# Kernel optimization log

Measured on AMD Instinct MI355X. Metric: run time of the kernel, lower is better.

## Reference

```python
import jax, jax.numpy as jnp
import numpy as np

N_NODES = 100000


def gcn_conv(x, edge_index, W, b):
    # PyG GCNConv: add self-loops, symmetric deg^-1/2 normalization,
    # linear transform, scatter-add aggregation onto destination nodes.
    src = edge_index[0]
    dst = edge_index[1]
    loops = jnp.arange(N_NODES, dtype=edge_index.dtype)
    src = jnp.concatenate([src, loops])
    dst = jnp.concatenate([dst, loops])
    deg = jax.ops.segment_sum(jnp.ones_like(src, dtype=x.dtype), dst,
                              num_segments=N_NODES)
    dinv = jnp.where(deg > 0, jax.lax.rsqrt(deg), 0.0)  # deg^-1/2, 0 for isolated
    norm = dinv[src] * dinv[dst]                        # [E+N]
    h = x @ W                                           # [N, out]
    msg = h[src] * norm[:, None]                        # [E+N, out]
    out = jax.ops.segment_sum(msg, dst, num_segments=N_NODES)
    return out + b


def setup_inputs() -> dict:
    key = jax.random.key(0)
    k1, k2, k3, k4, k5, k6 = jax.random.split(key, 6)
    in_c, hid_c, out_c = 128, 64, 40
    n_edges = 1_600_000
    x = jax.random.normal(k1, (N_NODES, in_c), dtype=jnp.float32)
    edge_index = jax.random.randint(k2, (2, n_edges), 0, N_NODES, dtype=jnp.int32)
    # Glorot-style init like GCNConv.reset_parameters
    W1 = jax.random.normal(k3, (in_c, hid_c), dtype=jnp.float32) * (1.0 / np.sqrt(in_c))
    b1 = jnp.zeros((hid_c,), dtype=jnp.float32)
    W2 = jax.random.normal(k4, (hid_c, out_c), dtype=jnp.float32) * (1.0 / np.sqrt(hid_c))
    b2 = jnp.zeros((out_c,), dtype=jnp.float32)
    return {"x": x, "edge_index": edge_index, "W1": W1, "b1": b1, "W2": W2, "b2": b2}


def reference(x, edge_index, W1, b1, W2, b2):
    h = jax.nn.relu(gcn_conv(x, edge_index, W1, b1))
    h = gcn_conv(h, edge_index, W2, b2)
    return jax.nn.log_softmax(h, axis=1)
```

## Files before the change

kernel.cpp:

```cpp
#include <hip/hip_runtime.h>
#include <math.h>

#define N_IN  128
#define N_HID 64
#define N_OUT 40

#define BSH   9
#define SZB   512
#define MAXBK 256
#define CAP   9216

typedef __attribute__((ext_vector_type(4))) float f32x4;
typedef __attribute__((ext_vector_type(8))) short bf16x8;

__device__ __forceinline__ unsigned short bf16_of(float x) {
    unsigned b = __float_as_uint(x);
    return (unsigned short)((b + 0x7fffu + ((b >> 16) & 1u)) >> 16);
}
__device__ __forceinline__ unsigned pack_bf16(float lo, float hi) {
    unsigned bl = __float_as_uint(lo), bh = __float_as_uint(hi);
    bl = (bl + 0x7fffu + ((bl >> 16) & 1u)) >> 16;
    bh = (bh + 0x7fffu + ((bh >> 16) & 1u)) & 0xffff0000u;
    return bl | bh;
}
__device__ __forceinline__ float bf_lo(unsigned u) { return __uint_as_float(u << 16); }
__device__ __forceinline__ float bf_hi(unsigned u) { return __uint_as_float(u & 0xffff0000u); }
__device__ __forceinline__ float2 bfup(unsigned u) { return make_float2(bf_lo(u), bf_hi(u)); }
__device__ __forceinline__ float2 f2add(float2 a, float2 b) { return make_float2(a.x + b.x, a.y + b.y); }

#define ACC8(u) { c0 = f2add(c0, bfup(u.x)); c1 = f2add(c1, bfup(u.y)); \
                  c2 = f2add(c2, bfup(u.z)); c3 = f2add(c3, bfup(u.w)); }

__global__ __launch_bounds__(256) void bucket_scatter2(const int* __restrict__ src,
                                                       const int* __restrict__ dst,
                                                       int E, int NBK,
                                                       int* __restrict__ bcnt,
                                                       int* __restrict__ ebuf) {
    __shared__ int h[MAXBK];
    __shared__ int base[MAXBK];
    int chunk = (E + gridDim.x - 1) / gridDim.x;
    int s = blockIdx.x * chunk;
    int e = min(E, s + chunk);
    for (int i = threadIdx.x; i < MAXBK; i += 256) h[i] = 0;
    __syncthreads();
    for (int i = s + threadIdx.x; i < e; i += 256)
        atomicAdd(&h[dst[i] >> BSH], 1);
    __syncthreads();
    for (int i = threadIdx.x; i < NBK; i += 256) {
        int c = h[i];
        base[i] = c ? atomicAdd(&bcnt[i], c) : 0;
    }
    __syncthreads();
    for (int i = threadIdx.x; i < MAXBK; i += 256) h[i] = 0;
    __syncthreads();
    for (int i = s + threadIdx.x; i < e; i += 256) {
        int d = dst[i];
        int b = d >> BSH;
        int lp = base[b] + atomicAdd(&h[b], 1);
        if (lp < CAP)
            ebuf[b * CAP + lp] = (src[i] << BSH) | (d & (SZB - 1));
    }
}

__global__ __launch_bounds__(256) void bucket_finalize2(const int* __restrict__ bcnt,
                                                        const int* __restrict__ ebuf,
                                                        int N,
                                                        int* __restrict__ off,
                                                        int* __restrict__ endo,
                                                        float* __restrict__ dinv,
                                                        int* __restrict__ ssrc) {
    __shared__ int deg[SZB];
    __shared__ int scn[SZB];
    __shared__ int cur[SZB];
    __shared__ int wsum[256];
    __shared__ int sstage[CAP];
    const int b   = blockIdx.x;
    const int cnt = min(bcnt[b], CAP);
    const int e0  = b * CAP;
    const int n0  = b << BSH;
    const int nn  = min(SZB, N - n0);
    const int t   = threadIdx.x;
    deg[t] = 0; deg[t + 256] = 0;
    __syncthreads();
    for (int i = t; i < cnt; i += 256)
        atomicAdd(&deg[ebuf[e0 + i] & (SZB - 1)], 1);
    __syncthreads();
    int a0 = deg[2 * t], a1 = deg[2 * t + 1];
    int v = a0 + a1;
    wsum[t] = v;
    __syncthreads();
    for (int o = 1; o < 256; o <<= 1) {
        int p = (t >= o) ? wsum[t - o] : 0;
        __syncthreads();
        wsum[t] += p;
        __syncthreads();
    }
    int ex = wsum[t] - v;
    scn[2 * t] = ex;       scn[2 * t + 1] = ex + a0;
    cur[2 * t] = ex;       cur[2 * t + 1] = ex + a0;
    __syncthreads();
    for (int i = t; i < nn; i += 256) {
        int st = e0 + scn[i];
        off[n0 + i]  = st;
        endo[n0 + i] = st + deg[i];
        dinv[n0 + i] = rsqrtf((float)(deg[i] + 1));
    }
    for (int i = t; i < cnt; i += 256) {
        int p = ebuf[e0 + i];
        int lp = atomicAdd(&cur[p & (SZB - 1)], 1);
        sstage[lp] = p >> BSH;
    }
    __syncthreads();
    for (int i = t; i < cnt; i += 256) ssrc[e0 + i] = sstage[i];
}

__global__ __launch_bounds__(256) void gemm1_mfma(const float* __restrict__ X,
                                                  const float* __restrict__ W,
                                                  const float* __restrict__ dinv,
                                                  unsigned* __restrict__ T, int nrows) {
    __shared__ unsigned xlds[8192];
    __shared__ unsigned wlds[4096];
    const int t    = threadIdx.x;
    const int row0 = blockIdx.x * 128;

#pragma unroll
    for (int i = 0; i < 16; ++i) {
        int idx = t + i * 256;
        int row = idx >> 5;
        int c4  = idx & 31;
        int gr = row0 + row;
        float4 v = make_float4(0.f, 0.f, 0.f, 0.f);
        if (gr < nrows) v = *(const float4*)&X[(long long)gr * 128 + c4 * 4];
        unsigned p0 = pack_bf16(v.x, v.y);
        unsigned p1 = pack_bf16(v.z, v.w);
        int byte = (row * 256 + c4 * 8) ^ ((row & 7) << 4);
        *(uint2*)((char*)xlds + byte) = make_uint2(p0, p1);
    }
    for (int i = t; i < 128 * 64; i += 256) {
        int k = i >> 6, c = i & 63;
        unsigned short hb = bf16_of(W[i]);
        int byte = (c * 256 + k * 2) ^ ((c & 7) << 4);
        *(unsigned short*)((char*)wlds + byte) = hb;
    }
    __syncthreads();

    const int w    = t >> 6;
    const int l    = t & 63;
    const int lrow = l & 15;
    const int lk   = l >> 4;

    f32x4 acc[2][4];
#pragma unroll
    for (int rt = 0; rt < 2; ++rt)
#pragma unroll
        for (int ct = 0; ct < 4; ++ct) acc[rt][ct] = (f32x4)0.f;

#pragma unroll
    for (int ks = 0; ks < 4; ++ks) {
        bf16x8 af[2], bfr[4];
#pragma unroll
        for (int rt = 0; rt < 2; ++rt) {
            int row = 32 * w + rt * 16 + lrow;
            int byte = (row * 256 + ks * 64 + lk * 16) ^ ((row & 7) << 4);
            af[rt] = *(bf16x8*)((char*)xlds + byte);
        }
#pragma unroll
        for (int ct = 0; ct < 4; ++ct) {
            int col = ct * 16 + lrow;
            int byte = (col * 256 + ks * 64 + lk * 16) ^ ((col & 7) << 4);
            bfr[ct] = *(bf16x8*)((char*)wlds + byte);
        }
#pragma unroll
        for (int rt = 0; rt < 2; ++rt)
#pragma unroll
            for (int ct = 0; ct < 4; ++ct)
                acc[rt][ct] = __builtin_amdgcn_mfma_f32_16x16x32_bf16(
                    af[rt], bfr[ct], acc[rt][ct], 0, 0, 0);
    }
    __syncthreads();
    float* ot = (float*)xlds;
#pragma unroll
    for (int rt = 0; rt < 2; ++rt)
#pragma unroll
        for (int ct = 0; ct < 4; ++ct)
#pragma unroll
            for (int i = 0; i < 4; ++i) {
                int row = 32 * w + rt * 16 + (l >> 4) * 4 + i;
                int col = ct * 16 + (l & 15);
                ot[row * 64 + col] = acc[rt][ct][i];
            }
    __syncthreads();
#pragma unroll
    for (int i = 0; i < 16; ++i) {
        int idx = t + i * 256;
        int row = idx >> 5, u = idx & 31;
        int gr = row0 + row;
        if (gr < nrows) {
            float2 v = *(float2*)&ot[row * 64 + u * 2];
            float dv = dinv[gr];
            T[(long long)gr * 32 + u] = pack_bf16(v.x * dv, v.y * dv);
        }
    }
}

__global__ __launch_bounds__(256) void agg_relu8(const int* __restrict__ off,
                                                 const int* __restrict__ endo,
                                                 const int* __restrict__ ssrc,
                                                 const float* __restrict__ dinv,
                                                 const unsigned* __restrict__ tab,
                                                 const float* __restrict__ bias,
                                                 unsigned* __restrict__ tabC, int N) {
    int node = blockIdx.x * 4 + (threadIdx.x >> 6);
    int lane = threadIdx.x & 63;
    if (node >= N) return;
    const int o  = lane >> 3;
    const int ln = lane & 7;
    int start = off[node], end = endo[node];
    float2 c0 = make_float2(0.f, 0.f), c1 = c0, c2 = c0, c3 = c0;
    for (int j = start; j < end; j += 64) {
        int idx = j + lane;
        int sidx = (idx < end) ? ssrc[idx] : 0;
        int cnt = min(64, end - j);
        int t = 0;
        for (; t + 16 <= cnt; t += 16) {
            int sA = __shfl(sidx, t + o);
            int sB = __shfl(sidx, t + 8 + o);
            uint4 uA = *(const uint4*)(tab + (long long)sA * 32 + 4 * ln);
            uint4 uB = *(const uint4*)(tab + (long long)sB * 32 + 4 * ln);
            ACC8(uA); ACC8(uB);
        }
        for (; t + 8 <= cnt; t += 8) {
            int s = __shfl(sidx, t + o);
            uint4 u = *(const uint4*)(tab + (long long)s * 32 + 4 * ln);
            ACC8(u);
        }
        if (t < cnt) {
            int ei = t + o;
            int s = __shfl(sidx, ei & 63);
            if (ei < cnt) {
                uint4 u = *(const uint4*)(tab + (long long)s * 32 + 4 * ln);
                ACC8(u);
            }
        }
    }
#pragma unroll
    for (int d = 8; d < 64; d <<= 1) {
        c0.x += __shfl_xor(c0.x, d); c0.y += __shfl_xor(c0.y, d);
        c1.x += __shfl_xor(c1.x, d); c1.y += __shfl_xor(c1.y, d);
        c2.x += __shfl_xor(c2.x, d); c2.y += __shfl_xor(c2.y, d);
        c3.x += __shfl_xor(c3.x, d); c3.y += __shfl_xor(c3.y, d);
    }
    if (o == 0) {
        uint4 us = *(const uint4*)(tab + (long long)node * 32 + 4 * ln);
        ACC8(us);
        float dd = dinv[node];
        float4 bb0 = *(const float4*)&bias[8 * ln];
        float4 bb1 = *(const float4*)&bias[8 * ln + 4];
        float v0 = fmaxf(c0.x * dd + bb0.x, 0.f);
        float v1 = fmaxf(c0.y * dd + bb0.y, 0.f);
        float v2 = fmaxf(c1.x * dd + bb0.z, 0.f);
        float v3 = fmaxf(c1.y * dd + bb0.w, 0.f);
        float v4 = fmaxf(c2.x * dd + bb1.x, 0.f);
        float v5 = fmaxf(c2.y * dd + bb1.y, 0.f);
        float v6 = fmaxf(c3.x * dd + bb1.z, 0.f);
        float v7 = fmaxf(c3.y * dd + bb1.w, 0.f);
        uint4 ot;
        ot.x = pack_bf16(v0 * dd, v1 * dd);
        ot.y = pack_bf16(v2 * dd, v3 * dd);
        ot.z = pack_bf16(v4 * dd, v5 * dd);
        ot.w = pack_bf16(v6 * dd, v7 * dd);
        *(uint4*)(tabC + (long long)node * 32 + 4 * ln) = ot;
    }
}

__global__ __launch_bounds__(256) void agg_g8(const int* __restrict__ off,
                                              const int* __restrict__ endo,
                                              const int* __restrict__ ssrc,
                                              const unsigned* __restrict__ tabC,
                                              unsigned* __restrict__ tabG, int N) {
    int node = blockIdx.x * 4 + (threadIdx.x >> 6);
    int lane = threadIdx.x & 63;
    if (node >= N) return;
    const int o  = lane >> 3;
    const int ln = lane & 7;
    int start = off[node], end = endo[node];
    float2 c0 = make_float2(0.f, 0.f), c1 = c0, c2 = c0, c3 = c0;
    for (int j = start; j < end; j += 64) {
        int idx = j + lane;
        int sidx = (idx < end) ? ssrc[idx] : 0;
        int cnt = min(64, end - j);
        int t = 0;
        for (; t + 16 <= cnt; t += 16) {
            int sA = __shfl(sidx, t + o);
            int sB = __shfl(sidx, t + 8 + o);
            uint4 uA = *(const uint4*)(tabC + (long long)sA * 32 + 4 * ln);
            uint4 uB = *(const uint4*)(tabC + (long long)sB * 32 + 4 * ln);
            ACC8(uA); ACC8(uB);
        }
        for (; t + 8 <= cnt; t += 8) {
            int s = __shfl(sidx, t + o);
            uint4 u = *(const uint4*)(tabC + (long long)s * 32 + 4 * ln);
            ACC8(u);
        }
        if (t < cnt) {
            int ei = t + o;
            int s = __shfl(sidx, ei & 63);
            if (ei < cnt) {
                uint4 u = *(const uint4*)(tabC + (long long)s * 32 + 4 * ln);
                ACC8(u);
            }
        }
    }
#pragma unroll
    for (int d = 8; d < 64; d <<= 1) {
        c0.x += __shfl_xor(c0.x, d); c0.y += __shfl_xor(c0.y, d);
        c1.x += __shfl_xor(c1.x, d); c1.y += __shfl_xor(c1.y, d);
        c2.x += __shfl_xor(c2.x, d); c2.y += __shfl_xor(c2.y, d);
        c3.x += __shfl_xor(c3.x, d); c3.y += __shfl_xor(c3.y, d);
    }
    if (o == 0) {
        uint4 us = *(const uint4*)(tabC + (long long)node * 32 + 4 * ln);
        ACC8(us);
        uint4 ot;
        ot.x = pack_bf16(c0.x, c0.y);
        ot.y = pack_bf16(c1.x, c1.y);
        ot.z = pack_bf16(c2.x, c2.y);
        ot.w = pack_bf16(c3.x, c3.y);
        *(uint4*)(tabG + (long long)node * 32 + 4 * ln) = ot;
    }
}

__global__ __launch_bounds__(256) void gemm2_mfma(const unsigned* __restrict__ tabG,
                                                  const float* __restrict__ W2,
                                                  const float* __restrict__ b2,
                                                  const float* __restrict__ dinv,
                                                  float* __restrict__ outp, int nrows) {
    __shared__ unsigned glds[4096];
    __shared__ unsigned wlds[1536];
    const int t    = threadIdx.x;
    const int row0 = blockIdx.x * 128;

#pragma unroll
    for (int i = 0; i < 4; ++i) {
        int idx = t + i * 256;
        int row = idx >> 3;
        int c4  = idx & 7;
        int gr = row0 + row;
        uint4 v = make_uint4(0, 0, 0, 0);
        if (gr < nrows) v = *(const uint4*)(tabG + (long long)gr * 32 + c4 * 4);
        int byte = (row * 128 + c4 * 16) ^ ((row & 7) << 4);
        *(uint4*)((char*)glds + byte) = v;
    }
    for (int i = t; i < 48 * 64; i += 256) {
        int c = i >> 6, k = i & 63;
        unsigned short hb = (c < N_OUT) ? bf16_of(W2[k * N_OUT + c]) : (unsigned short)0;
        int byte = (c * 128 + k * 2) ^ ((c & 7) << 4);
        *(unsigned short*)((char*)wlds + byte) = hb;
    }
    __syncthreads();

    const int w    = t >> 6;
    const int l    = t & 63;
    const int lrow = l & 15;
    const int lk   = l >> 4;

    f32x4 acc[2][3];
#pragma unroll
    for (int rt = 0; rt < 2; ++rt)
#pragma unroll
        for (int ct = 0; ct < 3; ++ct) acc[rt][ct] = (f32x4)0.f;

#pragma unroll
    for (int ks = 0; ks < 2; ++ks) {
        bf16x8 af[2], bfr[3];
#pragma unroll
        for (int rt = 0; rt < 2; ++rt) {
            int row = 32 * w + rt * 16 + lrow;
            int byte = (row * 128 + ks * 64 + lk * 16) ^ ((row & 7) << 4);
            af[rt] = *(bf16x8*)((char*)glds + byte);
        }
#pragma unroll
        for (int ct = 0; ct < 3; ++ct) {
            int col = ct * 16 + lrow;
            int byte = (col * 128 + ks * 64 + lk * 16) ^ ((col & 7) << 4);
            bfr[ct] = *(bf16x8*)((char*)wlds + byte);
        }
#pragma unroll
        for (int rt = 0; rt < 2; ++rt)
#pragma unroll
            for (int ct = 0; ct < 3; ++ct)
                acc[rt][ct] = __builtin_amdgcn_mfma_f32_16x16x32_bf16(
                    af[rt], bfr[ct], acc[rt][ct], 0, 0, 0);
    }

    const int q    = l >> 4;
    const int lcol = l & 15;
    float bb0 = b2[lcol];
    float bb1 = b2[16 + lcol];
    float bb2 = (lcol < 8) ? b2[32 + lcol] : 0.f;
#pragma unroll
    for (int rt = 0; rt < 2; ++rt)
#pragma unroll
        for (int i = 0; i < 4; ++i) {
            int rl = 32 * w + rt * 16 + q * 4 + i;
            int gr = row0 + rl;
            bool ok = gr < nrows;
            float dv = ok ? dinv[gr] : 0.f;
            float v0 = acc[rt][0][i] * dv + bb0;
            float v1 = acc[rt][1][i] * dv + bb1;
            float v2 = (lcol < 8) ? acc[rt][2][i] * dv + bb2 : -INFINITY;
            float m = fmaxf(fmaxf(v0, v1), v2);
            m = fmaxf(m, __shfl_xor(m, 1));
            m = fmaxf(m, __shfl_xor(m, 2));
            m = fmaxf(m, __shfl_xor(m, 4));
            m = fmaxf(m, __shfl_xor(m, 8));
            float ex = __expf(v0 - m) + __expf(v1 - m) + ((lcol < 8) ? __expf(v2 - m) : 0.f);
            ex += __shfl_xor(ex, 1);
            ex += __shfl_xor(ex, 2);
            ex += __shfl_xor(ex, 4);
            ex += __shfl_xor(ex, 8);
            float ls = logf(ex);
            if (ok) {
                long long base = (long long)gr * N_OUT;
                outp[base + lcol]      = v0 - m - ls;
                outp[base + 16 + lcol] = v1 - m - ls;
                if (lcol < 8) outp[base + 32 + lcol] = v2 - m - ls;
            }
        }
}

extern "C" void kernel_launch(void* const* d_in, const int* in_sizes, int n_in,
                              void* d_out, int out_size, void* d_ws, size_t ws_size,
                              hipStream_t stream) {
    const float* x  = (const float*)d_in[0];
    const int*   ei = (const int*)d_in[1];
    const float* W1 = (const float*)d_in[2];
    const float* b1 = (const float*)d_in[3];
    const float* W2 = (const float*)d_in[4];
    const float* b2 = (const float*)d_in[5];
    float* out = (float*)d_out;

    const int N = in_sizes[0] / N_IN;
    const int E = in_sizes[1] / 2;
    const int* src = ei;
    const int* dst = ei + E;
    const int NBK = (N + SZB - 1) >> BSH;

    int*      bcnt = (int*)d_ws;
    int*      off  = bcnt + MAXBK;
    int*      endo = off + N;
    float*    dinv = (float*)(endo + N);
    int*      ssrc = (int*)(dinv + N);
    unsigned* tabA = (unsigned*)(ssrc + (size_t)NBK * CAP);
    unsigned* tabC = tabA + (size_t)N * 32;
    unsigned* tabG = tabC + (size_t)N * 32;
    int*      ebuf = (int*)tabA;

    hipMemsetAsync(bcnt, 0, MAXBK * sizeof(int), stream);

    bucket_scatter2<<<512, 256, 0, stream>>>(src, dst, E, NBK, bcnt, ebuf);
    bucket_finalize2<<<NBK, 256, 0, stream>>>(bcnt, ebuf, N, off, endo, dinv, ssrc);

    gemm1_mfma<<<(N + 127) / 128, 256, 0, stream>>>(x, W1, dinv, tabA, N);
    agg_relu8<<<(N + 3) / 4, 256, 0, stream>>>(off, endo, ssrc, dinv, tabA, b1, tabC, N);

    agg_g8<<<(N + 3) / 4, 256, 0, stream>>>(off, endo, ssrc, tabC, tabG, N);
    gemm2_mfma<<<(N + 127) / 128, 256, 0, stream>>>(tabG, W2, b2, dinv, out, N);
}
```

Before: 179.0 us.

## Sort nodes by degree within buckets and aggregate with 8 lanes per node

The finalize kernel now counting-sorts nodes by in-degree inside each 512-node bucket and writes a packed per-node record (start, end, node id, dinv). Both aggregation kernels switch from one 64-lane wavefront per node, with shuffles and cross-lane reductions, to 8 lanes per node, 8 nodes per wavefront. Each 8-lane group walks its own edges two at a time, and wavefront divergence stays low because neighbouring nodes have similar degree. This removes the shuffle reductions and the idle lanes on low-degree nodes. The cost is less memory-level parallelism per node and extra sorting work in finalize.

```diff
diff --git a/kernel.cpp b/kernel.cpp
--- a/kernel.cpp
+++ b/kernel.cpp
@@ -65,14 +65,14 @@
 __global__ __launch_bounds__(256) void bucket_finalize2(const int* __restrict__ bcnt,
                                                         const int* __restrict__ ebuf,
                                                         int N,
-                                                        int* __restrict__ off,
-                                                        int* __restrict__ endo,
                                                         float* __restrict__ dinv,
-                                                        int* __restrict__ ssrc) {
+                                                        int* __restrict__ ssrc,
+                                                        int4* __restrict__ sinfo) {
     __shared__ int deg[SZB];
     __shared__ int scn[SZB];
     __shared__ int cur[SZB];
     __shared__ int wsum[256];
+    __shared__ int db[128];
     __shared__ int sstage[CAP];
     const int b   = blockIdx.x;
     const int cnt = min(bcnt[b], CAP);
@@ -99,11 +99,30 @@
     scn[2 * t] = ex;       scn[2 * t + 1] = ex + a0;
     cur[2 * t] = ex;       cur[2 * t + 1] = ex + a0;
     __syncthreads();
+    for (int i = t; i < nn; i += 256)
+        dinv[n0 + i] = rsqrtf((float)(deg[i] + 1));
+    if (t < 128) db[t] = 0;
+    __syncthreads();
+    for (int i = t; i < nn; i += 256)
+        atomicAdd(&db[min(deg[i], 127)], 1);
+    __syncthreads();
+    int hv = (t < 128) ? db[t] : 0;
+    wsum[t] = hv;
+    __syncthreads();
+    for (int o = 1; o < 128; o <<= 1) {
+        int p = (t >= o) ? wsum[t - o] : 0;
+        __syncthreads();
+        wsum[t] += p;
+        __syncthreads();
+    }
+    if (t < 128) db[t] = wsum[t] - hv;
+    __syncthreads();
     for (int i = t; i < nn; i += 256) {
+        int dg = deg[i];
+        int r  = atomicAdd(&db[min(dg, 127)], 1);
         int st = e0 + scn[i];
-        off[n0 + i]  = st;
-        endo[n0 + i] = st + deg[i];
-        dinv[n0 + i] = rsqrtf((float)(deg[i] + 1));
+        sinfo[n0 + r] = make_int4(st, st + dg, n0 + i,
+                                  __float_as_int(rsqrtf((float)(dg + 1))));
     }
     for (int i = t; i < cnt; i += 256) {
         int p = ebuf[e0 + i];
@@ -203,59 +222,33 @@
     }
 }
 
-__global__ __launch_bounds__(256) void agg_relu8(const int* __restrict__ off,
-                                                 const int* __restrict__ endo,
-                                                 const int* __restrict__ ssrc,
-                                                 const float* __restrict__ dinv,
-                                                 const unsigned* __restrict__ tab,
-                                                 const float* __restrict__ bias,
-                                                 unsigned* __restrict__ tabC, int N) {
-    int node = blockIdx.x * 4 + (threadIdx.x >> 6);
-    int lane = threadIdx.x & 63;
-    if (node >= N) return;
-    const int o  = lane >> 3;
-    const int ln = lane & 7;
-    int start = off[node], end = endo[node];
+__global__ __launch_bounds__(256) void agg_relu_o(const int4* __restrict__ sinfo,
+                                                  const int* __restrict__ ssrc,
+                                                  const unsigned* __restrict__ tab,
+                                                  const float* __restrict__ bias,
+                                                  unsigned* __restrict__ tabC, int N) {
+    int gidx = blockIdx.x * 32 + (threadIdx.x >> 3);
+    int ol   = threadIdx.x & 7;
+    int4 si = (gidx < N) ? sinfo[gidx] : make_int4(0, 0, 0, 0);
+    int j = si.x, end = si.y;
+    const unsigned* tp = tab + 4 * ol;
     float2 c0 = make_float2(0.f, 0.f), c1 = c0, c2 = c0, c3 = c0;
-    for (int j = start; j < end; j += 64) {
-        int idx = j + lane;
-        int sidx = (idx < end) ? ssrc[idx] : 0;
-        int cnt = min(64, end - j);
-        int t = 0;
-        for (; t + 16 <= cnt; t += 16) {
-            int sA = __shfl(sidx, t + o);
-            int sB = __shfl(sidx, t + 8 + o);
-            uint4 uA = *(const uint4*)(tab + (long long)sA * 32 + 4 * ln);
-            uint4 uB = *(const uint4*)(tab + (long long)sB * 32 + 4 * ln);
-            ACC8(uA); ACC8(uB);
-        }
-        for (; t + 8 <= cnt; t += 8) {
-            int s = __shfl(sidx, t + o);
-            uint4 u = *(const uint4*)(tab + (long long)s * 32 + 4 * ln);
-            ACC8(u);
-        }
-        if (t < cnt) {
-            int ei = t + o;
-            int s = __shfl(sidx, ei & 63);
-            if (ei < cnt) {
-                uint4 u = *(const uint4*)(tab + (long long)s * 32 + 4 * ln);
-                ACC8(u);
-            }
-        }
-    }
-#pragma unroll
-    for (int d = 8; d < 64; d <<= 1) {
-        c0.x += __shfl_xor(c0.x, d); c0.y += __shfl_xor(c0.y, d);
-        c1.x += __shfl_xor(c1.x, d); c1.y += __shfl_xor(c1.y, d);
-        c2.x += __shfl_xor(c2.x, d); c2.y += __shfl_xor(c2.y, d);
-        c3.x += __shfl_xor(c3.x, d); c3.y += __shfl_xor(c3.y, d);
-    }
-    if (o == 0) {
-        uint4 us = *(const uint4*)(tab + (long long)node * 32 + 4 * ln);
+    while (__any(j < end)) {
+        bool p0 = j < end, p1 = j + 1 < end;
+        int s0 = 0, s1 = 0;
+        if (p0) s0 = ssrc[j];
+        if (p1) s1 = ssrc[j + 1];
+        if (p0) { uint4 u = *(const uint4*)(tp + (long long)s0 * 32); ACC8(u); }
+        if (p1) { uint4 u = *(const uint4*)(tp + (long long)s1 * 32); ACC8(u); }
+        j += 2;
+    }
+    if (gidx < N) {
+        int node = si.z;
+        float dd = __int_as_float(si.w);
+        uint4 us = *(const uint4*)(tp + (long long)node * 32);
         ACC8(us);
-        float dd = dinv[node];
-        float4 bb0 = *(const float4*)&bias[8 * ln];
-        float4 bb1 = *(const float4*)&bias[8 * ln + 4];
+        float4 bb0 = *(const float4*)&bias[8 * ol];
+        float4 bb1 = *(const float4*)&bias[8 * ol + 4];
         float v0 = fmaxf(c0.x * dd + bb0.x, 0.f);
         float v1 = fmaxf(c0.y * dd + bb0.y, 0.f);
         float v2 = fmaxf(c1.x * dd + bb0.z, 0.f);
@@ -269,64 +262,39 @@
         ot.y = pack_bf16(v2 * dd, v3 * dd);
         ot.z = pack_bf16(v4 * dd, v5 * dd);
         ot.w = pack_bf16(v6 * dd, v7 * dd);
-        *(uint4*)(tabC + (long long)node * 32 + 4 * ln) = ot;
-    }
-}
-
-__global__ __launch_bounds__(256) void agg_g8(const int* __restrict__ off,
-                                              const int* __restrict__ endo,
-                                              const int* __restrict__ ssrc,
-                                              const unsigned* __restrict__ tabC,
-                                              unsigned* __restrict__ tabG, int N) {
-    int node = blockIdx.x * 4 + (threadIdx.x >> 6);
-    int lane = threadIdx.x & 63;
-    if (node >= N) return;
-    const int o  = lane >> 3;
-    const int ln = lane & 7;
-    int start = off[node], end = endo[node];
+        *(uint4*)(tabC + (long long)node * 32 + 4 * ol) = ot;
+    }
+}
+
+__global__ __launch_bounds__(256) void agg_g_o(const int4* __restrict__ sinfo,
+                                               const int* __restrict__ ssrc,
+                                               const unsigned* __restrict__ tabC,
+                                               unsigned* __restrict__ tabG, int N) {
+    int gidx = blockIdx.x * 32 + (threadIdx.x >> 3);
+    int ol   = threadIdx.x & 7;
+    int4 si = (gidx < N) ? sinfo[gidx] : make_int4(0, 0, 0, 0);
+    int j = si.x, end = si.y;
+    const unsigned* tp = tabC + 4 * ol;
     float2 c0 = make_float2(0.f, 0.f), c1 = c0, c2 = c0, c3 = c0;
-    for (int j = start; j < end; j += 64) {
-        int idx = j + lane;
-        int sidx = (idx < end) ? ssrc[idx] : 0;
-        int cnt = min(64, end - j);
-        int t = 0;
-        for (; t + 16 <= cnt; t += 16) {
-            int sA = __shfl(sidx, t + o);
-            int sB = __shfl(sidx, t + 8 + o);
-            uint4 uA = *(const uint4*)(tabC + (long long)sA * 32 + 4 * ln);
-            uint4 uB = *(const uint4*)(tabC + (long long)sB * 32 + 4 * ln);
-            ACC8(uA); ACC8(uB);
-        }
-        for (; t + 8 <= cnt; t += 8) {
-            int s = __shfl(sidx, t + o);
-            uint4 u = *(const uint4*)(tabC + (long long)s * 32 + 4 * ln);
-            ACC8(u);
-        }
-        if (t < cnt) {
-            int ei = t + o;
-            int s = __shfl(sidx, ei & 63);
-            if (ei < cnt) {
-                uint4 u = *(const uint4*)(tabC + (long long)s * 32 + 4 * ln);
-                ACC8(u);
-            }
-        }
-    }
-#pragma unroll
-    for (int d = 8; d < 64; d <<= 1) {
-        c0.x += __shfl_xor(c0.x, d); c0.y += __shfl_xor(c0.y, d);
-        c1.x += __shfl_xor(c1.x, d); c1.y += __shfl_xor(c1.y, d);
-        c2.x += __shfl_xor(c2.x, d); c2.y += __shfl_xor(c2.y, d);
-        c3.x += __shfl_xor(c3.x, d); c3.y += __shfl_xor(c3.y, d);
-    }
-    if (o == 0) {
-        uint4 us = *(const uint4*)(tabC + (long long)node * 32 + 4 * ln);
+    while (__any(j < end)) {
+        bool p0 = j < end, p1 = j + 1 < end;
+        int s0 = 0, s1 = 0;
+        if (p0) s0 = ssrc[j];
+        if (p1) s1 = ssrc[j + 1];
+        if (p0) { uint4 u = *(const uint4*)(tp + (long long)s0 * 32); ACC8(u); }
+        if (p1) { uint4 u = *(const uint4*)(tp + (long long)s1 * 32); ACC8(u); }
+        j += 2;
+    }
+    if (gidx < N) {
+        int node = si.z;
+        uint4 us = *(const uint4*)(tp + (long long)node * 32);
         ACC8(us);
         uint4 ot;
         ot.x = pack_bf16(c0.x, c0.y);
         ot.y = pack_bf16(c1.x, c1.y);
         ot.z = pack_bf16(c2.x, c2.y);
         ot.w = pack_bf16(c3.x, c3.y);
-        *(uint4*)(tabG + (long long)node * 32 + 4 * ln) = ot;
+        *(uint4*)(tabG + (long long)node * 32 + 4 * ol) = ot;
     }
 }
 
@@ -446,24 +414,23 @@
     const int* dst = ei + E;
     const int NBK = (N + SZB - 1) >> BSH;
 
-    int*      bcnt = (int*)d_ws;
-    int*      off  = bcnt + MAXBK;
-    int*      endo = off + N;
-    float*    dinv = (float*)(endo + N);
-    int*      ssrc = (int*)(dinv + N);
-    unsigned* tabA = (unsigned*)(ssrc + (size_t)NBK * CAP);
-    unsigned* tabC = tabA + (size_t)N * 32;
-    unsigned* tabG = tabC + (size_t)N * 32;
-    int*      ebuf = (int*)tabA;
+    int*      bcnt  = (int*)d_ws;
+    float*    dinv  = (float*)(bcnt + MAXBK);
+    int*      ssrc  = (int*)(dinv + N);
+    int4*     sinfo = (int4*)(ssrc + (size_t)NBK * CAP);
+    unsigned* tabA  = (unsigned*)(sinfo + N);
+    unsigned* tabC  = tabA + (size_t)N * 32;
+    unsigned* tabG  = tabC + (size_t)N * 32;
+    int*      ebuf  = (int*)tabA;
 
     hipMemsetAsync(bcnt, 0, MAXBK * sizeof(int), stream);
 
     bucket_scatter2<<<512, 256, 0, stream>>>(src, dst, E, NBK, bcnt, ebuf);
-    bucket_finalize2<<<NBK, 256, 0, stream>>>(bcnt, ebuf, N, off, endo, dinv, ssrc);
+    bucket_finalize2<<<NBK, 256, 0, stream>>>(bcnt, ebuf, N, dinv, ssrc, sinfo);
 
     gemm1_mfma<<<(N + 127) / 128, 256, 0, stream>>>(x, W1, dinv, tabA, N);
-    agg_relu8<<<(N + 3) / 4, 256, 0, stream>>>(off, endo, ssrc, dinv, tabA, b1, tabC, N);
-
-    agg_g8<<<(N + 3) / 4, 256, 0, stream>>>(off, endo, ssrc, tabC, tabG, N);
+    agg_relu_o<<<(N + 31) / 32, 256, 0, stream>>>(sinfo, ssrc, tabA, b1, tabC, N);
+
+    agg_g_o<<<(N + 31) / 32, 256, 0, stream>>>(sinfo, ssrc, tabC, tabG, N);
     gemm2_mfma<<<(N + 127) / 128, 256, 0, stream>>>(tabG, W2, b2, dinv, out, N);
 }
```

After: 187.0 us. 4.5% more time.
